# Performance work log

Measured on AMD Instinct MI355X. Metric: run time of the kernel, lower is better.

The kernel has to match this reference:

```python
import jax, jax.numpy as jnp
import numpy as np
import math

B, S, D = 4, 2048, 1024
H = 1
HD = D // H  # head_dim == hidden_dim since num_heads=1 (required by source's phase_encoder Linear)
HALF = HD // 2
SYNC_LOSS_WEIGHT = 0.01


def setup_inputs() -> dict:
    key = jax.random.key(0)
    ks = jax.random.split(key, 11)
    wstd = 0.02
    inp = {
        "x": jax.random.normal(ks[0], (B, S, D), dtype=jnp.float32),
        "Wq": jax.random.normal(ks[1], (D, D), dtype=jnp.float32) * wstd,
        "bq": jnp.zeros((D,), jnp.float32),
        "Wk": jax.random.normal(ks[2], (D, D), dtype=jnp.float32) * wstd,
        "bk": jnp.zeros((D,), jnp.float32),
        "Wv": jax.random.normal(ks[3], (D, D), dtype=jnp.float32) * wstd,
        "bv": jnp.zeros((D,), jnp.float32),
        "Wp": jax.random.normal(ks[4], (D, D), dtype=jnp.float32) * wstd,
        "bp": jnp.zeros((D,), jnp.float32),
        "Wo": jax.random.normal(ks[5], (D, D), dtype=jnp.float32) * wstd,
        "bo": jnp.zeros((D,), jnp.float32),
        "bifurcation_param": jnp.asarray(1.0, jnp.float32),
        "phase_coupling": jnp.asarray(0.5, jnp.float32),
    }
    return inp


def _phase(t, Wp, bp):
    # t: [B,H,S,HD] -> instantaneous phase via angle(complex(first_half, second_half))
    pf = t @ Wp.T + bp
    re, im = pf[..., :HALF], pf[..., HALF:]
    return jnp.arctan2(im, re)  # [B,H,S,HALF]


def reference(x, Wq, bq, Wk, bk, Wv, bv, Wp, bp, Wo, bo, bifurcation_param, phase_coupling):
    b, s, d = x.shape
    Q = (x @ Wq.T + bq).reshape(b, s, H, HD).transpose(0, 2, 1, 3)  # [B,H,S,HD]
    K = (x @ Wk.T + bk).reshape(b, s, H, HD).transpose(0, 2, 1, 3)
    V = (x @ Wv.T + bv).reshape(b, s, H, HD).transpose(0, 2, 1, 3)

    scores = jnp.einsum("bhqd,bhkd->bhqk", Q, K) / math.sqrt(HD)

    pQ = _phase(Q, Wp, bp)
    pK = _phase(K, Wp, bp)
    # mean_d cos(pQ - pK) == (cos(pQ)@cos(pK)^T + sin(pQ)@sin(pK)^T) / HALF
    sync = (jnp.einsum("bhqd,bhkd->bhqk", jnp.cos(pQ), jnp.cos(pK))
            + jnp.einsum("bhqd,bhkd->bhqk", jnp.sin(pQ), jnp.sin(pK))) / HALF

    t = jnp.tanh(scores)
    bif = bifurcation_param * t * (1.0 - t)

    chaotic = scores + phase_coupling * sync + bif
    attn = jax.nn.softmax(chaotic, axis=-1)

    av = jnp.einsum("bhqk,bhkd->bhqd", attn, V)
    av = av.transpose(0, 2, 1, 3).reshape(b, s, d)
    out = av @ Wo.T + bo

    # torch.var default: unbiased (ddof=1), over last dim of sync
    sync_loss = SYNC_LOSS_WEIGHT * jnp.var(sync, axis=-1, ddof=1).mean()
    return out, sync_loss
```

## Files before the change

kernel.cpp:

```cpp
#include <hip/hip_runtime.h>
#include <hip/hip_bf16.h>
#include <math.h>

#define S_LEN 2048
#define D_MODEL 1024
#define N_BATCH 4
#define N_HALF 512

typedef unsigned short u16;
typedef __attribute__((ext_vector_type(8))) short bf16x8;
typedef __attribute__((ext_vector_type(4))) float f32x4;

__device__ inline u16 f2bf(float v) {
  __hip_bfloat16 h = __float2bfloat16(v);
  return *reinterpret_cast<u16*>(&h);
}
__device__ inline float bf2f(u16 u) {
  __hip_bfloat16 h = *reinterpret_cast<__hip_bfloat16*>(&u);
  return __bfloat162float(h);
}
__device__ inline void gl2lds16(const void* g, void* l) {
  __builtin_amdgcn_global_load_lds(
      (const __attribute__((address_space(1))) unsigned int*)g,
      (__attribute__((address_space(3))) unsigned int*)l, 16, 0, 0);
}
__device__ inline float fast_tanh(float x) {
  float e = __expf(2.0f * x);
  return 1.0f - 2.0f / (e + 1.0f);
}

#define N0_X   (2097152LL)
#define NW_W   (262144LL)
__global__ __launch_bounds__(256)
void cast_bf4_multi(const float* __restrict__ sx, u16* __restrict__ dx,
                    const float* __restrict__ s1, u16* __restrict__ d1,
                    const float* __restrict__ s2, u16* __restrict__ d2,
                    const float* __restrict__ s3, u16* __restrict__ d3) {
  long long i = (long long)blockIdx.x * 256 + threadIdx.x;
  const float* s; u16* d; long long off;
  if (i < N0_X) { s = sx; d = dx; off = i; }
  else {
    long long k = i - N0_X;
    int w = (int)(k >> 18);
    off = k & (NW_W - 1);
    s = (w == 0) ? s1 : (w == 1) ? s2 : s3;
    d = (w == 0) ? d1 : (w == 1) ? d2 : d3;
  }
  float4 v = ((const float4*)s)[off];
  ushort4 o;
  o.x = f2bf(v.x); o.y = f2bf(v.y); o.z = f2bf(v.z); o.w = f2bf(v.w);
  ((ushort4*)d)[off] = o;
}
__global__ __launch_bounds__(256)
void cast_split(const float* __restrict__ src, u16* __restrict__ hi,
                u16* __restrict__ lo, long long n) {
  long long i = (long long)blockIdx.x * 256 + threadIdx.x;
  if (i < n) {
    float v = src[i];
    u16 h = f2bf(v);
    hi[i] = h;
    lo[i] = f2bf(v - bf2f(h));
  }
}
__global__ __launch_bounds__(256)
void transpose_split(const float* __restrict__ src, u16* __restrict__ hi,
                     u16* __restrict__ lo) {
  __shared__ float t[32][33];
  const int bx = blockIdx.x * 32;
  const int by = blockIdx.y * 32;
  const int c = threadIdx.x & 31;
  const int r0 = (threadIdx.x >> 5) * 4;
#pragma unroll
  for (int r = 0; r < 4; r++)
    t[r0 + r][c] = src[(long long)(by + r0 + r) * D_MODEL + bx + c];
  __syncthreads();
#pragma unroll
  for (int r = 0; r < 4; r++) {
    float v = t[c][r0 + r];
    long long idx = (long long)(bx + r0 + r) * D_MODEL + by + c;
    u16 h = f2bf(v);
    hi[idx] = h;
    lo[idx] = f2bf(v - bf2f(h));
  }
}
__global__ __launch_bounds__(256)
void w2_bias(const float* __restrict__ Wo, const float* __restrict__ bv,
             float* __restrict__ w2b) {
  const int d = blockIdx.x;
  const int tid = threadIdx.x;
  float acc = 0.f;
  for (int j = tid; j < D_MODEL; j += 256)
    acc += Wo[(long long)d * D_MODEL + j] * bv[j];
#pragma unroll
  for (int m = 1; m < 64; m <<= 1) acc += __shfl_xor(acc, m);
  __shared__ float red[4];
  if ((tid & 63) == 0) red[tid >> 6] = acc;
  __syncthreads();
  if (tid == 0) w2b[d] = red[0] + red[1] + red[2] + red[3];
}


__global__ __launch_bounds__(256, 2)
void qk_fused(const u16* __restrict__ X, const u16* __restrict__ Wq,
              const u16* __restrict__ Wk,
              const float* __restrict__ bq, const float* __restrict__ bk,
              u16* __restrict__ Qo, u16* __restrict__ Ko) {
  __shared__ u16 Xs[128 * 64];
  __shared__ u16 Qs[128 * 64];
  __shared__ u16 Ks[128 * 64];
  const int tid  = threadIdx.x;
  const int wave = tid >> 6;
  const int lane = tid & 63;
  const int quad = lane >> 4;
  const int tc   = lane & 15;
  const int bm = blockIdx.y * 128;
  const int bn = blockIdx.x * 128;
  const int wm = (wave & 1) * 64;
  const int wn = (wave >> 1) * 64;

  f32x4 acc1[4][4], acc2[4][4];
#pragma unroll
  for (int i = 0; i < 4; i++)
#pragma unroll
    for (int j = 0; j < 4; j++) {
      acc1[i][j] = (f32x4){0.f, 0.f, 0.f, 0.f};
      acc2[i][j] = (f32x4){0.f, 0.f, 0.f, 0.f};
    }

  const int srow8 = lane >> 3;
  const int scol  = ((lane & 7) ^ srow8) * 8;
  const int srowb = wave * 32;
  const u16* gx = X  + (long long)(bm + srowb + srow8) * D_MODEL + scol;
  const u16* gq = Wq + (long long)(bn + srowb + srow8) * D_MODEL + scol;
  const u16* gk = Wk + (long long)(bn + srowb + srow8) * D_MODEL + scol;
  const int wb = srowb * 64;
  const long long r8 = 8LL * D_MODEL;
  const int swzA = tc & 7;

  for (int k0 = 0; k0 < D_MODEL; k0 += 64) {
#pragma unroll
    for (int c = 0; c < 4; c++) {
      gl2lds16(gx + c * r8, Xs + wb + c * 512);
      gl2lds16(gq + c * r8, Qs + wb + c * 512);
      gl2lds16(gk + c * r8, Ks + wb + c * 512);
    }
    gx += 64; gq += 64; gk += 64;
    __syncthreads();
    bf16x8 af[4][2], bq4[4][2], bk4[4][2];
#pragma unroll
    for (int i = 0; i < 4; i++) {
      const int ra = (wm + i * 16 + tc) * 64;
      const int rb = (wn + i * 16 + tc) * 64;
#pragma unroll
      for (int ks = 0; ks < 2; ks++) {
        const int co = ((ks * 4 + quad) ^ swzA) * 8;
        af[i][ks]  = *(const bf16x8*)(Xs + ra + co);
        bq4[i][ks] = *(const bf16x8*)(Qs + rb + co);
        bk4[i][ks] = *(const bf16x8*)(Ks + rb + co);
      }
    }
#pragma unroll
    for (int i = 0; i < 4; i++)
#pragma unroll
      for (int j = 0; j < 4; j++) {
        acc1[i][j] = __builtin_amdgcn_mfma_f32_16x16x32_bf16(af[i][0], bq4[j][0], acc1[i][j], 0, 0, 0);
        acc2[i][j] = __builtin_amdgcn_mfma_f32_16x16x32_bf16(af[i][0], bk4[j][0], acc2[i][j], 0, 0, 0);
        acc1[i][j] = __builtin_amdgcn_mfma_f32_16x16x32_bf16(af[i][1], bq4[j][1], acc1[i][j], 0, 0, 0);
        acc2[i][j] = __builtin_amdgcn_mfma_f32_16x16x32_bf16(af[i][1], bk4[j][1], acc2[i][j], 0, 0, 0);
      }
    __syncthreads();
  }

#pragma unroll
  for (int i = 0; i < 4; i++) {
    const int row0 = bm + wm + i * 16 + quad * 4;
#pragma unroll
    for (int j = 0; j < 4; j++) {
      const int col = bn + wn + j * 16 + tc;
#pragma unroll
      for (int r = 0; r < 4; r++) {
        long long idx = (long long)(row0 + r) * D_MODEL + col;
        Qo[idx] = f2bf(acc1[i][j][r] + bq[col]);
        Ko[idx] = f2bf(acc2[i][j][r] + bk[col]);
      }
    }
  }
}

__global__ __launch_bounds__(256, 2)
void pf_fused(const u16* __restrict__ Qb, const u16* __restrict__ Wp,
              const float* __restrict__ bp,
              u16* __restrict__ pfQ, u16* __restrict__ pfK,
              long long TDo) {
  __shared__ u16 lds_all[3 * 128 * 64];
  u16* Qs = lds_all;
  u16* Ks = lds_all + 128 * 64;
  u16* Ws = lds_all + 2 * 128 * 64;
  const int tid  = threadIdx.x;
  const int wave = tid >> 6;
  const int lane = tid & 63;
  const int quad = lane >> 4;
  const int tc   = lane & 15;
  const int bm = blockIdx.y * 128;
  const int bn = blockIdx.x * 64;
  const int wm = (wave & 1) * 64;
  const int grp = wave >> 1;

  f32x4 acc1[4][4], acc2[4][4];
#pragma unroll
  for (int i = 0; i < 4; i++)
#pragma unroll
    for (int j = 0; j < 4; j++) {
      acc1[i][j] = (f32x4){0.f, 0.f, 0.f, 0.f};
      acc2[i][j] = (f32x4){0.f, 0.f, 0.f, 0.f};
    }

  const int srow8 = lane >> 3;
  const int scol  = ((lane & 7) ^ srow8) * 8;
  const int srowb = wave * 32;
  const u16* gq = Qb + (long long)(bm + srowb + srow8) * D_MODEL + scol;
  const u16* gk = gq + TDo;
  const u16* gw = Wp + (long long)(bn + srowb + srow8 + ((wave & 2) ? 448 : 0)) * D_MODEL + scol;
  const int wb = srowb * 64;
  const long long r8 = 8LL * D_MODEL;
  const int swzA = tc & 7;

  for (int k0 = 0; k0 < D_MODEL; k0 += 64) {
#pragma unroll
    for (int c = 0; c < 4; c++) {
      gl2lds16(gq + c * r8, Qs + wb + c * 512);
      gl2lds16(gk + c * r8, Ks + wb + c * 512);
      gl2lds16(gw + c * r8, Ws + wb + c * 512);
    }
    gq += 64; gk += 64; gw += 64;
    __syncthreads();
    bf16x8 aq[4][2], ak[4][2], bw[4][2];
    const int wn = grp * 64;
#pragma unroll
    for (int i = 0; i < 4; i++) {
      const int ra = (wm + i * 16 + tc) * 64;
      const int rb = (wn + i * 16 + tc) * 64;
#pragma unroll
      for (int ks = 0; ks < 2; ks++) {
        const int co = ((ks * 4 + quad) ^ swzA) * 8;
        aq[i][ks] = *(const bf16x8*)(Qs + ra + co);
        ak[i][ks] = *(const bf16x8*)(Ks + ra + co);
        bw[i][ks] = *(const bf16x8*)(Ws + rb + co);
      }
    }
#pragma unroll
    for (int i = 0; i < 4; i++)
#pragma unroll
      for (int j = 0; j < 4; j++) {
        acc1[i][j] = __builtin_amdgcn_mfma_f32_16x16x32_bf16(aq[i][0], bw[j][0], acc1[i][j], 0, 0, 0);
        acc2[i][j] = __builtin_amdgcn_mfma_f32_16x16x32_bf16(ak[i][0], bw[j][0], acc2[i][j], 0, 0, 0);
        acc1[i][j] = __builtin_amdgcn_mfma_f32_16x16x32_bf16(aq[i][1], bw[j][1], acc1[i][j], 0, 0, 0);
        acc2[i][j] = __builtin_amdgcn_mfma_f32_16x16x32_bf16(ak[i][1], bw[j][1], acc2[i][j], 0, 0, 0);
      }
    __syncthreads();
  }

  float* ex = (float*)lds_all;
  const long long colbase = (long long)bn + (long long)grp * 512;
#pragma unroll
  for (int o = 0; o < 2; o++) {
    u16* Ou = o ? pfK : pfQ;
#pragma unroll
    for (int half = 0; half < 2; half++) {
      int cnt = 0;
#pragma unroll
      for (int i = 2 * half; i < 2 * half + 2; i++)
#pragma unroll
        for (int j = 0; j < 4; j++) {
          f32x4 v = o ? acc2[i][j] : acc1[i][j];
          float b = bp[colbase + j * 16 + tc];
          v[0] += b; v[1] += b; v[2] += b; v[3] += b;
          *(f32x4*)(ex + wave * 2048 + cnt * 256 + lane * 4) = v;
          cnt++;
        }
      __syncthreads();
      cnt = 0;
#pragma unroll
      for (int i = 2 * half; i < 2 * half + 2; i++)
#pragma unroll
        for (int j = 0; j < 4; j++) {
          f32x4 own = *(const f32x4*)(ex + wave * 2048 + cnt * 256 + lane * 4);
          f32x4 oth = *(const f32x4*)(ex + (wave ^ 2) * 2048 + cnt * 256 + lane * 4);
          const int row0 = bm + wm + i * 16 + quad * 4;
          const long long col = colbase + j * 16 + tc;
#pragma unroll
          for (int r = 0; r < 4; r++) {
            float a = own[r], p = oth[r];
            float n2 = a * a + p * p;
            float outv = (grp == 0) ? 1.f : 0.f;
            if (n2 > 0.f) outv = a * (1.0f / sqrtf(n2));
            Ou[(long long)(row0 + r) * D_MODEL + col] = f2bf(outv);
          }
          cnt++;
        }
      __syncthreads();
    }
  }
}

__global__ __launch_bounds__(256)
void mfma_gemm_out3(const u16* __restrict__ Ah, const u16* __restrict__ Al,
                    const u16* __restrict__ Bh, const u16* __restrict__ Bl,
                    const float* __restrict__ bias, float* __restrict__ C,
                    int N, int K) {
  __shared__ u16 Ash[128 * 64];
  __shared__ u16 Asl[128 * 64];
  __shared__ u16 Bsh[128 * 64];
  __shared__ u16 Bsl[128 * 64];
  const int tid  = threadIdx.x;
  const int wave = tid >> 6;
  const int lane = tid & 63;
  const int quad = lane >> 4;
  const int tc   = lane & 15;
  const int bm = blockIdx.y * 128;
  const int bn = blockIdx.x * 128;
  const int wm = (wave & 1) * 64;
  const int wn = (wave >> 1) * 64;

  f32x4 acc[4][4];
#pragma unroll
  for (int i = 0; i < 4; i++)
#pragma unroll
    for (int j = 0; j < 4; j++) acc[i][j] = (f32x4){0.f, 0.f, 0.f, 0.f};

  const int srow8 = lane >> 3;
  const int scol  = ((lane & 7) ^ srow8) * 8;
  const int srowb = wave * 32;
  long long aoff = (long long)(bm + srowb + srow8) * K + scol;
  long long boff = (long long)(bn + srowb + srow8) * K + scol;
  const u16 *gah = Ah + aoff, *gal = Al + aoff;
  const u16 *gbh = Bh + boff, *gbl = Bl + boff;
  const int wb = srowb * 64;
  const long long r8K = 8LL * K;
  const int swzA = tc & 7;

  for (int k0 = 0; k0 < K; k0 += 64) {
#pragma unroll
    for (int c = 0; c < 4; c++) {
      gl2lds16(gah + c * r8K, Ash + wb + c * 512);
      gl2lds16(gal + c * r8K, Asl + wb + c * 512);
      gl2lds16(gbh + c * r8K, Bsh + wb + c * 512);
      gl2lds16(gbl + c * r8K, Bsl + wb + c * 512);
    }
    gah += 64; gal += 64; gbh += 64; gbl += 64;
    __syncthreads();
    bf16x8 ah[4][2], al[4][2], bh[4][2], bl[4][2];
#pragma unroll
    for (int i = 0; i < 4; i++) {
      const int ra = (wm + i * 16 + tc) * 64;
      const int rb = (wn + i * 16 + tc) * 64;
#pragma unroll
      for (int ks = 0; ks < 2; ks++) {
        const int co = ((ks * 4 + quad) ^ swzA) * 8;
        ah[i][ks] = *(const bf16x8*)(Ash + ra + co);
        al[i][ks] = *(const bf16x8*)(Asl + ra + co);
        bh[i][ks] = *(const bf16x8*)(Bsh + rb + co);
        bl[i][ks] = *(const bf16x8*)(Bsl + rb + co);
      }
    }
#pragma unroll
    for (int i = 0; i < 4; i++)
#pragma unroll
      for (int j = 0; j < 4; j++) {
#pragma unroll
        for (int ks = 0; ks < 2; ks++) {
          acc[i][j] = __builtin_amdgcn_mfma_f32_16x16x32_bf16(ah[i][ks], bh[j][ks], acc[i][j], 0, 0, 0);
          acc[i][j] = __builtin_amdgcn_mfma_f32_16x16x32_bf16(ah[i][ks], bl[j][ks], acc[i][j], 0, 0, 0);
          acc[i][j] = __builtin_amdgcn_mfma_f32_16x16x32_bf16(al[i][ks], bh[j][ks], acc[i][j], 0, 0, 0);
        }
      }
    __syncthreads();
  }
#pragma unroll
  for (int i = 0; i < 4; i++) {
    const int row0 = bm + wm + i * 16 + quad * 4;
#pragma unroll
    for (int j = 0; j < 4; j++) {
      const int col = bn + wn + j * 16 + tc;
      float b = bias ? bias[col] : 0.f;
#pragma unroll
      for (int r = 0; r < 4; r++)
        C[(long long)(row0 + r) * N + col] = acc[i][j][r] + b;
    }
  }
}

__global__ __launch_bounds__(256)
void vwt_kernel(const u16* __restrict__ W2h, const u16* __restrict__ W2l,
                const u16* __restrict__ X, const float* __restrict__ w2b,
                u16* __restrict__ Ch, u16* __restrict__ Cl,
                long long sB, long long sC) {
  __shared__ u16 Ah[128 * 64];
  __shared__ u16 Al[128 * 64];
  __shared__ u16 Bs[128 * 64];
  const int tid  = threadIdx.x;
  const int wave = tid >> 6;
  const int lane = tid & 63;
  const int quad = lane >> 4;
  const int tc   = lane & 15;
  const int bm = blockIdx.y * 128;
  const int bn = blockIdx.x * 128;
  const long long z = blockIdx.z;
  const int wm = (wave & 1) * 64;
  const int wn = (wave >> 1) * 64;

  f32x4 acc[4][4];
#pragma unroll
  for (int i = 0; i < 4; i++)
#pragma unroll
    for (int j = 0; j < 4; j++) acc[i][j] = (f32x4){0.f, 0.f, 0.f, 0.f};

  const int srow8 = lane >> 3;
  const int scol  = ((lane & 7) ^ srow8) * 8;
  const int srowb = wave * 32;
  const long long aoff = (long long)(bm + srowb + srow8) * D_MODEL + scol;
  const u16* gah = W2h + aoff;
  const u16* gal = W2l + aoff;
  const u16* gb  = X + z * sB + (long long)(bn + srowb + srow8) * D_MODEL + scol;
  const int wb = srowb * 64;
  const long long r8 = 8LL * D_MODEL;
  const int swzA = tc & 7;

  for (int k0 = 0; k0 < D_MODEL; k0 += 64) {
#pragma unroll
    for (int c = 0; c < 4; c++) {
      gl2lds16(gah + c * r8, Ah + wb + c * 512);
      gl2lds16(gal + c * r8, Al + wb + c * 512);
      gl2lds16(gb  + c * r8, Bs + wb + c * 512);
    }
    gah += 64; gal += 64; gb += 64;
    __syncthreads();
    bf16x8 ah4[4][2], al4[4][2], bx[4][2];
#pragma unroll
    for (int i = 0; i < 4; i++) {
      const int ra = (wm + i * 16 + tc) * 64;
      const int rb = (wn + i * 16 + tc) * 64;
#pragma unroll
      for (int ks = 0; ks < 2; ks++) {
        const int co = ((ks * 4 + quad) ^ swzA) * 8;
        ah4[i][ks] = *(const bf16x8*)(Ah + ra + co);
        al4[i][ks] = *(const bf16x8*)(Al + ra + co);
        bx[i][ks]  = *(const bf16x8*)(Bs + rb + co);
      }
    }
#pragma unroll
    for (int i = 0; i < 4; i++)
#pragma unroll
      for (int j = 0; j < 4; j++) {
        acc[i][j] = __builtin_amdgcn_mfma_f32_16x16x32_bf16(ah4[i][0], bx[j][0], acc[i][j], 0, 0, 0);
        acc[i][j] = __builtin_amdgcn_mfma_f32_16x16x32_bf16(al4[i][0], bx[j][0], acc[i][j], 0, 0, 0);
        acc[i][j] = __builtin_amdgcn_mfma_f32_16x16x32_bf16(ah4[i][1], bx[j][1], acc[i][j], 0, 0, 0);
        acc[i][j] = __builtin_amdgcn_mfma_f32_16x16x32_bf16(al4[i][1], bx[j][1], acc[i][j], 0, 0, 0);
      }
    __syncthreads();
  }

  u16* Chz = Ch + z * sC;
  u16* Clz = Cl + z * sC;
#pragma unroll
  for (int i = 0; i < 4; i++) {
    const int row0 = bm + wm + i * 16 + quad * 4;
#pragma unroll
    for (int j = 0; j < 4; j++) {
      const int col = bn + wn + j * 16 + tc;
#pragma unroll
      for (int r = 0; r < 4; r++) {
        float v = acc[i][j][r] + w2b[row0 + r];
        long long idx = (long long)(row0 + r) * S_LEN + col;
        u16 h = f2bf(v);
        Chz[idx] = h;
        Clz[idx] = f2bf(v - bf2f(h));
      }
    }
  }
}

__global__ __launch_bounds__(256)
void gemm_bsplit(const u16* __restrict__ A,
                 const u16* __restrict__ Bh, const u16* __restrict__ Bl,
                 const float* __restrict__ bias, float* __restrict__ C,
                 int N, int K, long long sA, long long sB, long long sC) {
  __shared__ u16 As[128 * 64];
  __shared__ u16 Bsh[128 * 64];
  __shared__ u16 Bsl[128 * 64];
  const int tid  = threadIdx.x;
  const int wave = tid >> 6;
  const int lane = tid & 63;
  const int quad = lane >> 4;
  const int tc   = lane & 15;
  const int bm = blockIdx.y * 128;
  const int bn = blockIdx.x * 128;
  const long long z = blockIdx.z;
  const int wm = (wave & 1) * 64;
  const int wn = (wave >> 1) * 64;

  f32x4 acc[4][4];
#pragma unroll
  for (int i = 0; i < 4; i++)
#pragma unroll
    for (int j = 0; j < 4; j++) acc[i][j] = (f32x4){0.f, 0.f, 0.f, 0.f};

  const int srow8 = lane >> 3;
  const int scol  = ((lane & 7) ^ srow8) * 8;
  const int srowb = wave * 32;
  const long long boff = (long long)(bn + srowb + srow8) * K + scol;
  const u16* ga  = A + z * sA + (long long)(bm + srowb + srow8) * K + scol;
  const u16* gbh = Bh + z * sB + boff;
  const u16* gbl = Bl + z * sB + boff;
  const int wb = srowb * 64;
  const long long r8K = 8LL * K;
  const int swzA = tc & 7;

  for (int k0 = 0; k0 < K; k0 += 64) {
#pragma unroll
    for (int c = 0; c < 4; c++) {
      gl2lds16(ga  + c * r8K, As  + wb + c * 512);
      gl2lds16(gbh + c * r8K, Bsh + wb + c * 512);
      gl2lds16(gbl + c * r8K, Bsl + wb + c * 512);
    }
    ga += 64; gbh += 64; gbl += 64;
    __syncthreads();
    bf16x8 af[4][2], bh[4][2], bl[4][2];
#pragma unroll
    for (int i = 0; i < 4; i++) {
      const int ra = (wm + i * 16 + tc) * 64;
      const int rb = (wn + i * 16 + tc) * 64;
#pragma unroll
      for (int ks = 0; ks < 2; ks++) {
        const int co = ((ks * 4 + quad) ^ swzA) * 8;
        af[i][ks] = *(const bf16x8*)(As  + ra + co);
        bh[i][ks] = *(const bf16x8*)(Bsh + rb + co);
        bl[i][ks] = *(const bf16x8*)(Bsl + rb + co);
      }
    }
#pragma unroll
    for (int i = 0; i < 4; i++)
#pragma unroll
      for (int j = 0; j < 4; j++) {
        acc[i][j] = __builtin_amdgcn_mfma_f32_16x16x32_bf16(af[i][0], bh[j][0], acc[i][j], 0, 0, 0);
        acc[i][j] = __builtin_amdgcn_mfma_f32_16x16x32_bf16(af[i][0], bl[j][0], acc[i][j], 0, 0, 0);
        acc[i][j] = __builtin_amdgcn_mfma_f32_16x16x32_bf16(af[i][1], bh[j][1], acc[i][j], 0, 0, 0);
        acc[i][j] = __builtin_amdgcn_mfma_f32_16x16x32_bf16(af[i][1], bl[j][1], acc[i][j], 0, 0, 0);
      }
    __syncthreads();
  }

  float* Cz = C + z * sC;
#pragma unroll
  for (int i = 0; i < 4; i++) {
    const int row0 = bm + wm + i * 16 + quad * 4;
#pragma unroll
    for (int j = 0; j < 4; j++) {
      const int col = bn + wn + j * 16 + tc;
#pragma unroll
      for (int r = 0; r < 4; r++)
        Cz[(long long)(row0 + r) * N + col] = acc[i][j][r] + bias[col];
    }
  }
}

__global__ __launch_bounds__(256, 2)
void chaotic_fused(const u16* __restrict__ Q, const u16* __restrict__ Kt,
                   const u16* __restrict__ Uq, const u16* __restrict__ Uk,
                   float* __restrict__ Cc,
                   float* __restrict__ ssum, float* __restrict__ ssq,
                   const float* __restrict__ bifp, const float* __restrict__ pcp) {
  __shared__ u16 Qs[128 * 64];
  __shared__ u16 Ks[128 * 64];
  __shared__ u16 Us[128 * 64];
  __shared__ u16 Ws[128 * 64];
  const int tid  = threadIdx.x;
  const int wave = tid >> 6;
  const int lane = tid & 63;
  const int quad = lane >> 4;
  const int tc   = lane & 15;
  const int bm = blockIdx.y * 128;
  const int bn = blockIdx.x * 128;
  const long long z = blockIdx.z;
  const long long sQ = (long long)S_LEN * D_MODEL;
  const int wm = (wave & 1) * 64;
  const int wn = (wave >> 1) * 64;

  f32x4 acc1[4][4], acc2[4][4];
#pragma unroll
  for (int i = 0; i < 4; i++)
#pragma unroll
    for (int j = 0; j < 4; j++) {
      acc1[i][j] = (f32x4){0.f, 0.f, 0.f, 0.f};
      acc2[i][j] = (f32x4){0.f, 0.f, 0.f, 0.f};
    }

  const int srow8  = lane >> 3;
  const int scol   = ((lane & 7) ^ srow8) * 8;
  const int srowb  = wave * 32;
  const u16* gq = Q  + z * sQ + (long long)(bm + srowb + srow8) * D_MODEL + scol;
  const u16* gk = Kt + z * sQ + (long long)(bn + srowb + srow8) * D_MODEL + scol;
  const u16* gu = Uq + z * sQ + (long long)(bm + srowb + srow8) * D_MODEL + scol;
  const u16* gw = Uk + z * sQ + (long long)(bn + srowb + srow8) * D_MODEL + scol;
  const int wb = srowb * 64;
  const long long r8 = 8LL * D_MODEL;

  const int swzA = tc & 7;

  for (int k0 = 0; k0 < D_MODEL; k0 += 64) {
#pragma unroll
    for (int c = 0; c < 4; c++) {
      gl2lds16(gq + c * r8, Qs + wb + c * 512);
      gl2lds16(gk + c * r8, Ks + wb + c * 512);
      gl2lds16(gu + c * r8, Us + wb + c * 512);
      gl2lds16(gw + c * r8, Ws + wb + c * 512);
    }
    gq += 64; gk += 64; gu += 64; gw += 64;
    __syncthreads();
    {
      bf16x8 af[4][2], bg[4][2];
#pragma unroll
      for (int i = 0; i < 4; i++) {
        const int ra = (wm + i * 16 + tc) * 64;
        const int rb = (wn + i * 16 + tc) * 64;
#pragma unroll
        for (int ks = 0; ks < 2; ks++) {
          const int co = ((ks * 4 + quad) ^ swzA) * 8;
          af[i][ks] = *(const bf16x8*)(Qs + ra + co);
          bg[i][ks] = *(const bf16x8*)(Ks + rb + co);
        }
      }
#pragma unroll
      for (int i = 0; i < 4; i++)
#pragma unroll
        for (int j = 0; j < 4; j++) {
          acc1[i][j] = __builtin_amdgcn_mfma_f32_16x16x32_bf16(af[i][0], bg[j][0], acc1[i][j], 0, 0, 0);
          acc1[i][j] = __builtin_amdgcn_mfma_f32_16x16x32_bf16(af[i][1], bg[j][1], acc1[i][j], 0, 0, 0);
        }
    }
    {
      bf16x8 cf[4][2], dg[4][2];
#pragma unroll
      for (int i = 0; i < 4; i++) {
        const int ra = (wm + i * 16 + tc) * 64;
        const int rb = (wn + i * 16 + tc) * 64;
#pragma unroll
        for (int ks = 0; ks < 2; ks++) {
          const int co = ((ks * 4 + quad) ^ swzA) * 8;
          cf[i][ks] = *(const bf16x8*)(Us + ra + co);
          dg[i][ks] = *(const bf16x8*)(Ws + rb + co);
        }
      }
#pragma unroll
      for (int i = 0; i < 4; i++)
#pragma unroll
        for (int j = 0; j < 4; j++) {
          acc2[i][j] = __builtin_amdgcn_mfma_f32_16x16x32_bf16(cf[i][0], dg[j][0], acc2[i][j], 0, 0, 0);
          acc2[i][j] = __builtin_amdgcn_mfma_f32_16x16x32_bf16(cf[i][1], dg[j][1], acc2[i][j], 0, 0, 0);
        }
    }
    __syncthreads();
  }

  const float bif = *bifp;
  const float pc  = *pcp;
  float rsum[4][4], rsq[4][4];
#pragma unroll
  for (int i = 0; i < 4; i++)
#pragma unroll
    for (int r = 0; r < 4; r++) { rsum[i][r] = 0.f; rsq[i][r] = 0.f; }

  float* C = Cc + z * (long long)S_LEN * S_LEN;
#pragma unroll
  for (int i = 0; i < 4; i++) {
    const int row0 = bm + wm + i * 16 + quad * 4;
#pragma unroll
    for (int j = 0; j < 4; j++) {
      const int col = bn + wn + j * 16 + tc;
#pragma unroll
      for (int r = 0; r < 4; r++) {
        float sc = acc1[i][j][r] * 0.03125f;
        float sy = acc2[i][j][r] * (1.0f / 512.0f);
        float t  = fast_tanh(sc);
        C[(long long)(row0 + r) * S_LEN + col] = sc + pc * sy + bif * t * (1.0f - t);
        rsum[i][r] += sy;
        rsq[i][r]  += sy * sy;
      }
    }
  }
#pragma unroll
  for (int m = 1; m < 16; m <<= 1) {
#pragma unroll
    for (int i = 0; i < 4; i++)
#pragma unroll
      for (int r = 0; r < 4; r++) {
        rsum[i][r] += __shfl_xor(rsum[i][r], m);
        rsq[i][r]  += __shfl_xor(rsq[i][r], m);
      }
  }
  if (tc == 0) {
#pragma unroll
    for (int i = 0; i < 4; i++)
#pragma unroll
      for (int r = 0; r < 4; r++) {
        long long rr = z * S_LEN + bm + wm + i * 16 + quad * 4 + r;
        atomicAdd(&ssum[rr], rsum[i][r]);
        atomicAdd(&ssq[rr],  rsq[i][r]);
      }
  }
}

__global__ __launch_bounds__(256)
void softmax_bf(const float* __restrict__ Cc, u16* __restrict__ P) {
  const long long row = (long long)blockIdx.y * S_LEN + blockIdx.x;
  const float* p = Cc + row * S_LEN;
  u16* q = P + row * S_LEN;
  const int tid = threadIdx.x;
  float v[8];
  float m = -3.402823466e+38f;
#pragma unroll
  for (int i = 0; i < 8; i++) { v[i] = p[tid + i * 256]; m = fmaxf(m, v[i]); }
#pragma unroll
  for (int mask = 1; mask < 64; mask <<= 1) m = fmaxf(m, __shfl_xor(m, mask));
  __shared__ float red[8];
  if ((tid & 63) == 0) red[tid >> 6] = m;
  __syncthreads();
  m = fmaxf(fmaxf(red[0], red[1]), fmaxf(red[2], red[3]));
  float s = 0.f;
#pragma unroll
  for (int i = 0; i < 8; i++) { v[i] = __expf(v[i] - m); s += v[i]; }
#pragma unroll
  for (int mask = 1; mask < 64; mask <<= 1) s += __shfl_xor(s, mask);
  __syncthreads();
  if ((tid & 63) == 0) red[4 + (tid >> 6)] = s;
  __syncthreads();
  s = red[4] + red[5] + red[6] + red[7];
  float inv = 1.0f / s;
#pragma unroll
  for (int i = 0; i < 8; i++) q[tid + i * 256] = f2bf(v[i] * inv);
}

__global__ __launch_bounds__(1024)
void syncloss_kernel(const float* __restrict__ ssum, const float* __restrict__ ssq,
                     float* __restrict__ out) {
  const int tid = threadIdx.x;
  float acc = 0.f;
  for (int r = tid; r < N_BATCH * S_LEN; r += 1024) {
    float su = ssum[r], sq = ssq[r];
    acc += (sq - su * su * (1.0f / 2048.0f)) * (1.0f / 2047.0f);
  }
#pragma unroll
  for (int mask = 1; mask < 64; mask <<= 1) acc += __shfl_xor(acc, mask);
  __shared__ float red[16];
  if ((tid & 63) == 0) red[tid >> 6] = acc;
  __syncthreads();
  if (tid == 0) {
    float t = 0.f;
#pragma unroll
    for (int k = 0; k < 16; k++) t += red[k];
    out[0] = 0.01f * (t / (float)(N_BATCH * S_LEN));
  }
}

extern "C" void kernel_launch(void* const* d_in, const int* in_sizes, int n_in,
                              void* d_out, int out_size, void* d_ws, size_t ws_size,
                              hipStream_t stream) {
  const float* x    = (const float*)d_in[0];
  const float* Wq   = (const float*)d_in[1];
  const float* bq   = (const float*)d_in[2];
  const float* Wk   = (const float*)d_in[3];
  const float* bk   = (const float*)d_in[4];
  const float* Wv   = (const float*)d_in[5];
  const float* bv   = (const float*)d_in[6];
  const float* Wp   = (const float*)d_in[7];
  const float* bp   = (const float*)d_in[8];
  const float* Wo   = (const float*)d_in[9];
  const float* bo   = (const float*)d_in[10];
  const float* bifp = (const float*)d_in[11];
  const float* pcp  = (const float*)d_in[12];
  float* out = (float*)d_out;

  const long long NROW = (long long)N_BATCH * S_LEN;
  const long long TD   = NROW * D_MODEL;
  const long long WSZ  = (long long)D_MODEL * D_MODEL;

  u16* xbf   = (u16*)d_ws;
  u16* wqb   = xbf + TD;
  u16* wkb   = wqb + WSZ;
  u16* wpb   = wkb + WSZ;
  u16* woh   = wpb + WSZ;
  u16* wol   = woh + WSZ;
  u16* wvth  = wol + WSZ;
  u16* wvtl  = wvth + WSZ;
  u16* w2h   = wvtl + WSZ;
  u16* w2l   = w2h + WSZ;
  float* W2f = (float*)(w2l + WSZ);
  float* w2b = W2f + WSZ;
  u16* Qbf   = (u16*)(w2b + D_MODEL);
  u16* Kbf   = Qbf + TD;
  u16* pfQ   = Kbf + TD;
  u16* pfK   = pfQ + TD;
  float* Cc  = (float*)(pfK + TD);
  float* ssum = Cc + (long long)N_BATCH * S_LEN * S_LEN;
  float* ssq  = ssum + NROW;
  u16* attn = Qbf;
  u16* vwh  = pfQ;
  u16* vwl  = pfK;

  dim3 blk(256);
  const long long sQ = (long long)S_LEN * D_MODEL;
  const long long sS = (long long)S_LEN * S_LEN;

  cast_bf4_multi<<<11264, blk, 0, stream>>>(x, xbf, Wq, wqb, Wk, wkb, Wp, wpb);
  cast_split<<<(int)(WSZ / 256), blk, 0, stream>>>(Wo, woh, wol, WSZ);
  transpose_split<<<dim3(32, 32), blk, 0, stream>>>(Wv, wvth, wvtl);
  mfma_gemm_out3<<<dim3(8, 8, 1), blk, 0, stream>>>(
      woh, wol, wvth, wvtl, nullptr, W2f, D_MODEL, D_MODEL);
  cast_split<<<(int)(WSZ / 256), blk, 0, stream>>>(W2f, w2h, w2l, WSZ);
  w2_bias<<<D_MODEL, blk, 0, stream>>>(Wo, bv, w2b);

  qk_fused<<<dim3(8, 64), blk, 0, stream>>>(xbf, wqb, wkb, bq, bk, Qbf, Kbf);
  pf_fused<<<dim3(8, 64), blk, 0, stream>>>(Qbf, wpb, bp, pfQ, pfK, TD);
  hipMemsetAsync(ssum, 0, (size_t)(2 * NROW) * sizeof(float), stream);

  chaotic_fused<<<dim3(16, 16, N_BATCH), blk, 0, stream>>>(
      Qbf, Kbf, pfQ, pfK, Cc, ssum, ssq, bifp, pcp);
  vwt_kernel<<<dim3(16, 8, N_BATCH), blk, 0, stream>>>(
      w2h, w2l, xbf, w2b, vwh, vwl, sQ, sQ);
  softmax_bf<<<dim3(S_LEN, N_BATCH), blk, 0, stream>>>(Cc, attn);
  gemm_bsplit<<<dim3(8, 16, N_BATCH), blk, 0, stream>>>(
      attn, vwh, vwl, bo, out,
      D_MODEL, S_LEN, sS, sQ, sQ);
  syncloss_kernel<<<1, 1024, 0, stream>>>(ssum, ssq, out + TD);
}
```

Measured before the change: 487.4 us.

## Double-buffer LDS tiles with BK=32 in split GEMM and fused chaotic kernel

Converts the single-buffered BK=64 K-loop in gemm_bsplit and chaotic_fused into a double-buffered BK=32 pipeline. The next tile is prefetched via global_load_lds while MFMAs run on the current one, using explicit vmcnt waits and raw s_barrier. The goal is to hide global-load latency behind compute. In exchange there are twice as many barriers per K, a new swizzle pattern for the 32-wide rows, and hand-counted vmcnt values that must match the number of outstanding loads.

```diff
diff --git a/kernel.cpp b/kernel.cpp
--- a/kernel.cpp
+++ b/kernel.cpp
@@ -485,9 +485,9 @@
                  const u16* __restrict__ Bh, const u16* __restrict__ Bl,
                  const float* __restrict__ bias, float* __restrict__ C,
                  int N, int K, long long sA, long long sB, long long sC) {
-  __shared__ u16 As[128 * 64];
-  __shared__ u16 Bsh[128 * 64];
-  __shared__ u16 Bsl[128 * 64];
+  __shared__ u16 As[2][128 * 32];
+  __shared__ u16 Bsh[2][128 * 32];
+  __shared__ u16 Bsl[2][128 * 32];
   const int tid  = threadIdx.x;
   const int wave = tid >> 6;
   const int lane = tid & 63;
@@ -505,49 +505,61 @@
 #pragma unroll
     for (int j = 0; j < 4; j++) acc[i][j] = (f32x4){0.f, 0.f, 0.f, 0.f};
 
-  const int srow8 = lane >> 3;
-  const int scol  = ((lane & 7) ^ srow8) * 8;
-  const int srowb = wave * 32;
-  const long long boff = (long long)(bn + srowb + srow8) * K + scol;
-  const u16* ga  = A + z * sA + (long long)(bm + srowb + srow8) * K + scol;
+  const int srow16 = lane >> 2;
+  const int scol   = (((lane & 3) ^ ((lane >> 3) & 3))) * 8;
+  const int srowb  = wave * 32;
+  const long long boff = (long long)(bn + srowb + srow16) * K + scol;
+  const u16* ga  = A + z * sA + (long long)(bm + srowb + srow16) * K + scol;
   const u16* gbh = Bh + z * sB + boff;
   const u16* gbl = Bl + z * sB + boff;
-  const int wb = srowb * 64;
-  const long long r8K = 8LL * K;
-  const int swzA = tc & 7;
-
-  for (int k0 = 0; k0 < K; k0 += 64) {
-#pragma unroll
-    for (int c = 0; c < 4; c++) {
-      gl2lds16(ga  + c * r8K, As  + wb + c * 512);
-      gl2lds16(gbh + c * r8K, Bsh + wb + c * 512);
-      gl2lds16(gbl + c * r8K, Bsl + wb + c * 512);
-    }
-    ga += 64; gbh += 64; gbl += 64;
-    __syncthreads();
-    bf16x8 af[4][2], bh[4][2], bl[4][2];
+  const int wb = srowb * 32;
+  const long long r16K = 16LL * K;
+  const int swz = (tc >> 1) & 3;
+  const int NT = K >> 5;
+
+#pragma unroll
+  for (int c = 0; c < 2; c++) {
+    gl2lds16(ga  + c * r16K, As[0]  + wb + c * 512);
+    gl2lds16(gbh + c * r16K, Bsh[0] + wb + c * 512);
+    gl2lds16(gbl + c * r16K, Bsl[0] + wb + c * 512);
+  }
+  ga += 32; gbh += 32; gbl += 32;
+
+  for (int t = 0; t < NT; ++t) {
+    const int cur = t & 1, nxt = cur ^ 1;
+    if (t < NT - 1) {
+#pragma unroll
+      for (int c = 0; c < 2; c++) {
+        gl2lds16(ga  + c * r16K, As[nxt]  + wb + c * 512);
+        gl2lds16(gbh + c * r16K, Bsh[nxt] + wb + c * 512);
+        gl2lds16(gbl + c * r16K, Bsl[nxt] + wb + c * 512);
+      }
+      ga += 32; gbh += 32; gbl += 32;
+      asm volatile("s_waitcnt vmcnt(6)" ::: "memory");
+    } else {
+      asm volatile("s_waitcnt vmcnt(0)" ::: "memory");
+    }
+    __builtin_amdgcn_s_barrier();
+    __builtin_amdgcn_sched_barrier(0);
+    bf16x8 af[4], bh[4], bl[4];
+    const int co = (quad ^ swz) * 8;
 #pragma unroll
     for (int i = 0; i < 4; i++) {
-      const int ra = (wm + i * 16 + tc) * 64;
-      const int rb = (wn + i * 16 + tc) * 64;
-#pragma unroll
-      for (int ks = 0; ks < 2; ks++) {
-        const int co = ((ks * 4 + quad) ^ swzA) * 8;
-        af[i][ks] = *(const bf16x8*)(As  + ra + co);
-        bh[i][ks] = *(const bf16x8*)(Bsh + rb + co);
-        bl[i][ks] = *(const bf16x8*)(Bsl + rb + co);
-      }
+      const int ra = (wm + i * 16 + tc) * 32 + co;
+      const int rb = (wn + i * 16 + tc) * 32 + co;
+      af[i] = *(const bf16x8*)(As[cur]  + ra);
+      bh[i] = *(const bf16x8*)(Bsh[cur] + rb);
+      bl[i] = *(const bf16x8*)(Bsl[cur] + rb);
     }
 #pragma unroll
     for (int i = 0; i < 4; i++)
 #pragma unroll
       for (int j = 0; j < 4; j++) {
-        acc[i][j] = __builtin_amdgcn_mfma_f32_16x16x32_bf16(af[i][0], bh[j][0], acc[i][j], 0, 0, 0);
-        acc[i][j] = __builtin_amdgcn_mfma_f32_16x16x32_bf16(af[i][0], bl[j][0], acc[i][j], 0, 0, 0);
-        acc[i][j] = __builtin_amdgcn_mfma_f32_16x16x32_bf16(af[i][1], bh[j][1], acc[i][j], 0, 0, 0);
-        acc[i][j] = __builtin_amdgcn_mfma_f32_16x16x32_bf16(af[i][1], bl[j][1], acc[i][j], 0, 0, 0);
-      }
-    __syncthreads();
+        acc[i][j] = __builtin_amdgcn_mfma_f32_16x16x32_bf16(af[i], bh[j], acc[i][j], 0, 0, 0);
+        acc[i][j] = __builtin_amdgcn_mfma_f32_16x16x32_bf16(af[i], bl[j], acc[i][j], 0, 0, 0);
+      }
+    __builtin_amdgcn_sched_barrier(0);
+    __builtin_amdgcn_s_barrier();
   }
 
   float* Cz = C + z * sC;
@@ -570,10 +582,10 @@
                    float* __restrict__ Cc,
                    float* __restrict__ ssum, float* __restrict__ ssq,
                    const float* __restrict__ bifp, const float* __restrict__ pcp) {
-  __shared__ u16 Qs[128 * 64];
-  __shared__ u16 Ks[128 * 64];
-  __shared__ u16 Us[128 * 64];
-  __shared__ u16 Ws[128 * 64];
+  __shared__ u16 Qs[2][128 * 32];
+  __shared__ u16 Ks[2][128 * 32];
+  __shared__ u16 Us[2][128 * 32];
+  __shared__ u16 Ws[2][128 * 32];
   const int tid  = threadIdx.x;
   const int wave = tid >> 6;
   const int lane = tid & 63;
@@ -595,71 +607,72 @@
       acc2[i][j] = (f32x4){0.f, 0.f, 0.f, 0.f};
     }
 
-  const int srow8  = lane >> 3;
-  const int scol   = ((lane & 7) ^ srow8) * 8;
+  const int srow16 = lane >> 2;
+  const int scol   = (((lane & 3) ^ ((lane >> 3) & 3))) * 8;
   const int srowb  = wave * 32;
-  const u16* gq = Q  + z * sQ + (long long)(bm + srowb + srow8) * D_MODEL + scol;
-  const u16* gk = Kt + z * sQ + (long long)(bn + srowb + srow8) * D_MODEL + scol;
-  const u16* gu = Uq + z * sQ + (long long)(bm + srowb + srow8) * D_MODEL + scol;
-  const u16* gw = Uk + z * sQ + (long long)(bn + srowb + srow8) * D_MODEL + scol;
-  const int wb = srowb * 64;
-  const long long r8 = 8LL * D_MODEL;
-
-  const int swzA = tc & 7;
-
-  for (int k0 = 0; k0 < D_MODEL; k0 += 64) {
-#pragma unroll
-    for (int c = 0; c < 4; c++) {
-      gl2lds16(gq + c * r8, Qs + wb + c * 512);
-      gl2lds16(gk + c * r8, Ks + wb + c * 512);
-      gl2lds16(gu + c * r8, Us + wb + c * 512);
-      gl2lds16(gw + c * r8, Ws + wb + c * 512);
-    }
-    gq += 64; gk += 64; gu += 64; gw += 64;
-    __syncthreads();
+  const u16* gq = Q  + z * sQ + (long long)(bm + srowb + srow16) * D_MODEL + scol;
+  const u16* gk = Kt + z * sQ + (long long)(bn + srowb + srow16) * D_MODEL + scol;
+  const u16* gu = Uq + z * sQ + (long long)(bm + srowb + srow16) * D_MODEL + scol;
+  const u16* gw = Uk + z * sQ + (long long)(bn + srowb + srow16) * D_MODEL + scol;
+  const int wb = srowb * 32;
+  const long long r16 = 16LL * D_MODEL;
+  const int swz = (tc >> 1) & 3;
+
+#pragma unroll
+  for (int c = 0; c < 2; c++) {
+    gl2lds16(gq + c * r16, Qs[0] + wb + c * 512);
+    gl2lds16(gk + c * r16, Ks[0] + wb + c * 512);
+    gl2lds16(gu + c * r16, Us[0] + wb + c * 512);
+    gl2lds16(gw + c * r16, Ws[0] + wb + c * 512);
+  }
+  gq += 32; gk += 32; gu += 32; gw += 32;
+
+  for (int t = 0; t < 32; ++t) {
+    const int cur = t & 1, nxt = cur ^ 1;
+    if (t < 31) {
+#pragma unroll
+      for (int c = 0; c < 2; c++) {
+        gl2lds16(gq + c * r16, Qs[nxt] + wb + c * 512);
+        gl2lds16(gk + c * r16, Ks[nxt] + wb + c * 512);
+        gl2lds16(gu + c * r16, Us[nxt] + wb + c * 512);
+        gl2lds16(gw + c * r16, Ws[nxt] + wb + c * 512);
+      }
+      gq += 32; gk += 32; gu += 32; gw += 32;
+      asm volatile("s_waitcnt vmcnt(8)" ::: "memory");
+    } else {
+      asm volatile("s_waitcnt vmcnt(0)" ::: "memory");
+    }
+    __builtin_amdgcn_s_barrier();
+    __builtin_amdgcn_sched_barrier(0);
+    const int co = (quad ^ swz) * 8;
     {
-      bf16x8 af[4][2], bg[4][2];
+      bf16x8 af[4], bg[4];
 #pragma unroll
       for (int i = 0; i < 4; i++) {
-        const int ra = (wm + i * 16 + tc) * 64;
-        const int rb = (wn + i * 16 + tc) * 64;
-#pragma unroll
-        for (int ks = 0; ks < 2; ks++) {
-          const int co = ((ks * 4 + quad) ^ swzA) * 8;
-          af[i][ks] = *(const bf16x8*)(Qs + ra + co);
-          bg[i][ks] = *(const bf16x8*)(Ks + rb + co);
-        }
+        af[i] = *(const bf16x8*)(Qs[cur] + (wm + i * 16 + tc) * 32 + co);
+        bg[i] = *(const bf16x8*)(Ks[cur] + (wn + i * 16 + tc) * 32 + co);
       }
 #pragma unroll
       for (int i = 0; i < 4; i++)
 #pragma unroll
-        for (int j = 0; j < 4; j++) {
-          acc1[i][j] = __builtin_amdgcn_mfma_f32_16x16x32_bf16(af[i][0], bg[j][0], acc1[i][j], 0, 0, 0);
-          acc1[i][j] = __builtin_amdgcn_mfma_f32_16x16x32_bf16(af[i][1], bg[j][1], acc1[i][j], 0, 0, 0);
-        }
+        for (int j = 0; j < 4; j++)
+          acc1[i][j] = __builtin_amdgcn_mfma_f32_16x16x32_bf16(af[i], bg[j], acc1[i][j], 0, 0, 0);
     }
     {
-      bf16x8 cf[4][2], dg[4][2];
+      bf16x8 cf[4], dg[4];
 #pragma unroll
       for (int i = 0; i < 4; i++) {
-        const int ra = (wm + i * 16 + tc) * 64;
-        const int rb = (wn + i * 16 + tc) * 64;
-#pragma unroll
-        for (int ks = 0; ks < 2; ks++) {
-          const int co = ((ks * 4 + quad) ^ swzA) * 8;
-          cf[i][ks] = *(const bf16x8*)(Us + ra + co);
-          dg[i][ks] = *(const bf16x8*)(Ws + rb + co);
-        }
+        cf[i] = *(const bf16x8*)(Us[cur] + (wm + i * 16 + tc) * 32 + co);
+        dg[i] = *(const bf16x8*)(Ws[cur] + (wn + i * 16 + tc) * 32 + co);
       }
 #pragma unroll
       for (int i = 0; i < 4; i++)
 #pragma unroll
-        for (int j = 0; j < 4; j++) {
-          acc2[i][j] = __builtin_amdgcn_mfma_f32_16x16x32_bf16(cf[i][0], dg[j][0], acc2[i][j], 0, 0, 0);
-          acc2[i][j] = __builtin_amdgcn_mfma_f32_16x16x32_bf16(cf[i][1], dg[j][1], acc2[i][j], 0, 0, 0);
-        }
-    }
-    __syncthreads();
+        for (int j = 0; j < 4; j++)
+          acc2[i][j] = __builtin_amdgcn_mfma_f32_16x16x32_bf16(cf[i], dg[j], acc2[i][j], 0, 0, 0);
+    }
+    __builtin_amdgcn_sched_barrier(0);
+    __builtin_amdgcn_s_barrier();
   }
 
   const float bif = *bifp;
```

Result: slower. 508.5 us (+4.3%).
